# Kernel optimization log

Measured on AMD Instinct MI355X. Metric: run time of the kernel, lower is better.

The kernel has to match this reference:

```python
import jax, jax.numpy as jnp
import numpy as np

N, C_IN, C_OUT, T, V, S = 32, 64, 64, 512, 25, 3
R = C_IN // 2  # rel_channels (in_channel not in (3,9) -> in//rel_reduction=2)
EPS = 1e-5


def setup_inputs() -> dict:
    key = jax.random.key(0)
    ks = jax.random.split(key, 14)
    p = lambda k, shape, s=0.05: jax.random.normal(k, shape, dtype=jnp.float32) * s
    return {
        "x": jax.random.normal(ks[0], (N, C_IN, T, V), dtype=jnp.float32),
        "A": p(ks[1], (S, V, V), 0.2),            # fixed adjacency per subset
        "w1": p(ks[2], (S, R, C_IN)),             # conv1 1x1 per subset
        "b1": p(ks[3], (S, R)),
        "w2": p(ks[4], (S, R, C_IN)),             # conv2 1x1
        "b2": p(ks[5], (S, R)),
        "w3": p(ks[6], (S, C_OUT, C_IN)),         # conv3 1x1 (value)
        "b3": p(ks[7], (S, C_OUT)),
        "w4": p(ks[8], (S, C_OUT, R)),            # conv4 1x1 on relation tensor
        "b4": p(ks[9], (S, C_OUT)),
        "alpha": p(ks[10], (S,), 0.1),            # per-subset scalar (nn.Parameter zeros(1); randomized for non-degenerate test)
        "bn_gamma": jnp.ones((C_OUT,), dtype=jnp.float32),
        "bn_beta": jnp.zeros((C_OUT,), dtype=jnp.float32),
    }


def reference(x, A, w1, b1, w2, b2, w3, b3, w4, b4, alpha, bn_gamma, bn_beta):
    # x: [N,C,T,V]. 1x1 conv commutes with mean over T, so pool first (same math).
    xm = x.mean(axis=2)                                              # [N,C,V]
    q = jnp.einsum('ncv,src->nsrv', xm, w1) + b1[None, :, :, None]   # conv1(x).mean(-2)
    k = jnp.einsum('ncv,src->nsrv', xm, w2) + b2[None, :, :, None]   # conv2(x).mean(-2)
    v = jnp.einsum('nctv,soc->nsotv', x, w3) + b3[None, :, :, None, None]  # conv3(x)
    # outer difference over nodes: [N,S,R,V,V]
    rel = jax.nn.relu(q[..., :, None] - k[..., None, :])
    # conv4 (1x1 over rel channels) * alpha + A[s]
    att = jnp.einsum('nsruv,sor->nsouv', rel, w4) + b4[None, :, :, None, None]
    att = att * alpha[None, :, None, None, None] + A[None, :, None, :, :]  # [N,S,O,V,V]
    # aggregation: einsum('ncuv,nctv->nctu') summed over subsets
    y = jnp.einsum('nsouv,nsotv->notu', att, v)                      # [N,O,T,V]
    # BatchNorm2d in training mode (batch statistics, biased variance)
    mu = y.mean(axis=(0, 2, 3), keepdims=True)
    var = y.var(axis=(0, 2, 3), keepdims=True)
    ybn = (y - mu) * jax.lax.rsqrt(var + EPS) * bn_gamma[None, :, None, None] + bn_beta[None, :, None, None]
    # act(y) + bn(y) + residual (Identity since in_channel == out_channel)
    return jax.nn.relu(y) + ybn + x
```

## Files before the change

kernel.cpp:

```cpp
#include <hip/hip_runtime.h>
#include <hip/hip_bf16.h>

#define XM_OFF   0
#define ATT_OFF  51200
#define SSUM_OFF 3891200
#define SSQ_OFF  3891264
#define SCL_OFF  3891328
#define SHF_OFF  3891392
#define Y_BYTE_OFF  (3891456ull * 4ull)
#define VT_BYTE_OFF (Y_BYTE_OFF + 52428800ull)

#define CONV_SWAP 0

typedef __attribute__((ext_vector_type(8))) short short8;
typedef __attribute__((ext_vector_type(4))) float f32x4;

__device__ __forceinline__ ushort f2bs(float f) {
  __hip_bfloat16 h = __float2bfloat16(f);
  ushort u; __builtin_memcpy(&u, &h, 2); return u;
}
__device__ __forceinline__ float bs2f(ushort u) {
  return __uint_as_float((unsigned)u << 16);
}

__global__ __launch_bounds__(256) void k_xm(const float* __restrict__ x,
                                            float* __restrict__ ws) {
  const int b = blockIdx.x;
  const int tid = threadIdx.x;
  if (b == 0 && tid < 128) ws[SSUM_OFF + tid] = 0.f;
  const float* base = x + (size_t)b * 12800;
  float acc[25];
#pragma unroll
  for (int v = 0; v < 25; ++v) acc[v] = 0.f;
  for (int t = tid; t < 512; t += 256) {
    const float* row = base + t * 25;
#pragma unroll
    for (int v = 0; v < 25; ++v) acc[v] += row[v];
  }
  __shared__ float red[256][25];
#pragma unroll
  for (int v = 0; v < 25; ++v) red[tid][v] = acc[v];
  __syncthreads();
  for (int st = 128; st > 0; st >>= 1) {
    if (tid < st) {
#pragma unroll
      for (int v = 0; v < 25; ++v) red[tid][v] += red[tid + st][v];
    }
    __syncthreads();
  }
  if (tid < 25) ws[XM_OFF + b * 25 + tid] = red[0][tid] * (1.0f / 512.0f);
}

__global__ __launch_bounds__(256) void k_att(const float* __restrict__ ws,
    const float* __restrict__ A, const float* __restrict__ w1, const float* __restrict__ b1,
    const float* __restrict__ w2, const float* __restrict__ b2, const float* __restrict__ w4,
    const float* __restrict__ b4, const float* __restrict__ alpha, float* __restrict__ attg) {
  const int b = blockIdx.x;
  const int n = b / 24; const int r = b % 24; const int s = r >> 3; const int og = r & 7;
  const int tid = threadIdx.x;
  __shared__ float xs[1600];
  __shared__ float qb[800];
  __shared__ float kb[800];
  for (int j = tid; j < 1600; j += 256) xs[j] = ws[XM_OFF + n * 1600 + j];
  __syncthreads();
  for (int i = tid; i < 1600; i += 256) {
    const int half = i / 800;
    const int ii = i % 800;
    const int rr = ii / 25, v = ii % 25;
    const float* w = half ? w2 : w1;
    const float* bb = half ? b2 : b1;
    float acc = bb[s * 32 + rr];
    const float* wr = w + (s * 32 + rr) * 64;
#pragma unroll 8
    for (int c = 0; c < 64; ++c) acc += wr[c] * xs[c * 25 + v];
    (half ? kb : qb)[ii] = acc;
  }
  __syncthreads();
  const float al = alpha[s];
  for (int i = tid; i < 5000; i += 256) {
    const int o2 = i / 625, r2 = i % 625;
    const int u = r2 / 25, v = r2 % 25;
    const int o = og * 8 + o2;
    const float* wr = w4 + (s * 64 + o) * 32;
    float acc = 0.f;
#pragma unroll 8
    for (int rr2 = 0; rr2 < 32; ++rr2) {
      const float d = qb[rr2 * 25 + u] - kb[rr2 * 25 + v];
      acc += wr[rr2] * fmaxf(d, 0.f);
    }
    attg[((size_t)(n * 3 + s) * 64 + o) * 625 + r2] =
        (acc + b4[s * 64 + o]) * al + A[s * 625 + r2];
  }
}

__global__ __launch_bounds__(256) void k_conv3(const float* __restrict__ x,
    const float* __restrict__ w3, const float* __restrict__ b3,
    ushort* __restrict__ vt, int n_base) {
  __shared__ ushort xbf[2][16][64][8];
  __shared__ ushort shv[64 * 256];
  const int tid = threadIdx.x;
  const int nh = blockIdx.x / 50, chunk = blockIdx.x % 50;
  const int n = n_base + nh;
  const int item0 = chunk * 256;

  {
    const float* xb = x + (size_t)n * 819200 + item0 + tid;
    const int col = tid & 15, nt = tid >> 4;
#pragma unroll
    for (int cq = 0; cq < 16; ++cq) {
      const int c0 = cq * 4;
      const float f0 = xb[(size_t)(c0 + 0) * 12800];
      const float f1 = xb[(size_t)(c0 + 1) * 12800];
      const float f2 = xb[(size_t)(c0 + 2) * 12800];
      const float f3 = xb[(size_t)(c0 + 3) * 12800];
      ushort4 p;
      p.x = f2bs(f0); p.y = f2bs(f1); p.z = f2bs(f2); p.w = f2bs(f3);
      const int kb = c0 >> 5;
#if CONV_SWAP == 0
      const int h  = (c0 >> 4) & 1;
      const int kg = (c0 >> 2) & 3;
      *(ushort4*)&xbf[kb][nt][kg * 16 + col][h * 4] = p;
#else
      const int cp = c0 & 31;
      *(ushort4*)&xbf[kb][nt][(cp >> 3) * 16 + col][c0 & 4] = p;
#endif
    }
  }
  __syncthreads();

  const int lane = tid & 63, wid = tid >> 6;
  const int o0 = wid * 16;
  const int orow = o0 + (lane & 15);
  const int kg = lane >> 4;

  short8 afr[3][2];
  float4 b3v[3];
#pragma unroll
  for (int s = 0; s < 3; ++s) {
    const float* wrow = w3 + ((size_t)s * 64 + orow) * 64;
#pragma unroll
    for (int kb2 = 0; kb2 < 2; ++kb2) {
#if CONV_SWAP == 0
      const float4 lo = *(const float4*)(wrow + kb2 * 32 + kg * 4);
      const float4 hi = *(const float4*)(wrow + kb2 * 32 + 16 + kg * 4);
#else
      const float4 lo = *(const float4*)(wrow + kb2 * 32 + kg * 8);
      const float4 hi = *(const float4*)(wrow + kb2 * 32 + kg * 8 + 4);
#endif
      short8 a;
      a[0] = (short)f2bs(lo.x); a[1] = (short)f2bs(lo.y);
      a[2] = (short)f2bs(lo.z); a[3] = (short)f2bs(lo.w);
      a[4] = (short)f2bs(hi.x); a[5] = (short)f2bs(hi.y);
      a[6] = (short)f2bs(hi.z); a[7] = (short)f2bs(hi.w);
      afr[s][kb2] = a;
    }
    b3v[s] = *(const float4*)(b3 + s * 64 + o0 + (lane >> 4) * 4);
  }

  const int obase = o0 + (lane >> 4) * 4;
  const int colit = lane & 15;

  for (int s = 0; s < 3; ++s) {
#pragma unroll
    for (int nt = 0; nt < 16; ++nt) {
      f32x4 acc;
      acc[0] = b3v[s].x; acc[1] = b3v[s].y; acc[2] = b3v[s].z; acc[3] = b3v[s].w;
      const short8 bf0 = *(const short8*)&xbf[0][nt][lane][0];
      const short8 bf1 = *(const short8*)&xbf[1][nt][lane][0];
      acc = __builtin_amdgcn_mfma_f32_16x16x32_bf16(afr[s][0], bf0, acc, 0, 0, 0);
      acc = __builtin_amdgcn_mfma_f32_16x16x32_bf16(afr[s][1], bf1, acc, 0, 0, 0);
      const int item = nt * 16 + colit;
#pragma unroll
      for (int r = 0; r < 4; ++r) {
        const int oo = obase + r;
        shv[oo * 256 + (item ^ ((oo & 7) << 3))] = f2bs(acc[r]);
      }
    }
    __syncthreads();
    {
      const int o = tid >> 2, seg = tid & 3;
      ushort* dst = vt + (((size_t)nh * 3 + s) * 64 + o) * 12800 + item0;
      const ushort* srow = &shv[o * 256];
      const int xr = (o & 7) << 3;
#pragma unroll
      for (int g = 0; g < 8; ++g) {
        const int ib = g * 32 + seg * 8;
        *(int4*)(dst + ib) = *(const int4*)(srow + (ib ^ xr));
      }
    }
    __syncthreads();
  }
}

__global__ __launch_bounds__(256) void k_agg(const ushort* __restrict__ vt,
    const float* __restrict__ attg, float* __restrict__ ssum, float* __restrict__ ssq,
    ushort* __restrict__ yg, int n_base) {
  const int bid = blockIdx.x;
  const int tc = bid & 1, o = (bid >> 1) & 63, nh = bid >> 7;
  const int n = n_base + nh;
  const int t = tc * 256 + threadIdx.x;
  const float* ab = attg + ((size_t)(n * 3) * 64 + o) * 625;
  float acc[25];
#pragma unroll
  for (int u = 0; u < 25; ++u) acc[u] = 0.f;

  for (int s = 0; s < 3; ++s) {
    const ushort* vr = vt + ((((size_t)nh * 3 + s) * 64 + o) * 512 + t) * 25;
    float xv[25];
#pragma unroll
    for (int v = 0; v < 25; ++v) xv[v] = bs2f(vr[v]);
    const float* ar = ab + s * 40000;
#pragma unroll
    for (int u = 0; u < 25; ++u) {
      const float* arr = ar + u * 25;
#pragma unroll
      for (int v = 0; v < 25; ++v) acc[u] = fmaf(arr[v], xv[v], acc[u]);
    }
  }

  ushort* yr = yg + (((size_t)n * 64 + o) * 512 + t) * 25;
  float s1 = 0.f, s2 = 0.f;
#pragma unroll
  for (int u = 0; u < 25; ++u) {
    const float yv = acc[u];
    s1 += yv; s2 += yv * yv;
    yr[u] = f2bs(yv);
  }
#pragma unroll
  for (int off = 32; off > 0; off >>= 1) {
    s1 += __shfl_down(s1, off);
    s2 += __shfl_down(s2, off);
  }
  __shared__ float rs[8];
  const int lane = threadIdx.x & 63, wid = threadIdx.x >> 6;
  if (lane == 0) { rs[wid] = s1; rs[4 + wid] = s2; }
  __syncthreads();
  if (threadIdx.x == 0) {
    atomicAdd(&ssum[o], rs[0] + rs[1] + rs[2] + rs[3]);
    atomicAdd(&ssq[o], rs[4] + rs[5] + rs[6] + rs[7]);
  }
}

__global__ __launch_bounds__(64) void k_stats(const float* __restrict__ ssum,
    const float* __restrict__ ssq, const float* __restrict__ gamma,
    const float* __restrict__ beta, float* __restrict__ scl, float* __restrict__ shf) {
  const int o = threadIdx.x;
  const float inv = 1.0f / 409600.0f;
  const float mu = ssum[o] * inv;
  const float var = ssq[o] * inv - mu * mu;
  const float rstd = rsqrtf(var + 1e-5f);
  const float sc = gamma[o] * rstd;
  scl[o] = sc;
  shf[o] = beta[o] - mu * sc;
}

__global__ __launch_bounds__(256) void k_final(const float* __restrict__ x,
    const ushort* __restrict__ yg, const float* __restrict__ scl,
    const float* __restrict__ shf, float* __restrict__ out) {
  const int stride = gridDim.x * blockDim.x;
  for (int i = blockIdx.x * 256 + threadIdx.x; i < 6553600; i += stride) {
    const int o = (i / 3200) & 63;
    const float sc = scl[o], sh = shf[o];
    const float4 xv = ((const float4*)x)[i];
    const ushort4 yu = ((const ushort4*)yg)[i];
    const float y0 = bs2f(yu.x), y1 = bs2f(yu.y), y2 = bs2f(yu.z), y3 = bs2f(yu.w);
    float4 r;
    r.x = fmaxf(y0, 0.f) + y0 * sc + sh + xv.x;
    r.y = fmaxf(y1, 0.f) + y1 * sc + sh + xv.y;
    r.z = fmaxf(y2, 0.f) + y2 * sc + sh + xv.z;
    r.w = fmaxf(y3, 0.f) + y3 * sc + sh + xv.w;
    ((float4*)out)[i] = r;
  }
}

extern "C" void kernel_launch(void* const* d_in, const int* in_sizes, int n_in,
                              void* d_out, int out_size, void* d_ws, size_t ws_size,
                              hipStream_t stream) {
  const float* x     = (const float*)d_in[0];
  const float* A     = (const float*)d_in[1];
  const float* w1    = (const float*)d_in[2];
  const float* b1    = (const float*)d_in[3];
  const float* w2    = (const float*)d_in[4];
  const float* b2    = (const float*)d_in[5];
  const float* w3    = (const float*)d_in[6];
  const float* b3    = (const float*)d_in[7];
  const float* w4    = (const float*)d_in[8];
  const float* b4    = (const float*)d_in[9];
  const float* alpha = (const float*)d_in[10];
  const float* gamma = (const float*)d_in[11];
  const float* beta  = (const float*)d_in[12];
  float* ws = (float*)d_ws;
  float* attg = ws + ATT_OFF;
  ushort* yg = (ushort*)((char*)d_ws + Y_BYTE_OFF);
  ushort* vtb = (ushort*)((char*)d_ws + VT_BYTE_OFF);
  float* out = (float*)d_out;

  k_xm<<<2048, 256, 0, stream>>>(x, ws);
  k_att<<<768, 256, 0, stream>>>(ws, A, w1, b1, w2, b2, w4, b4, alpha, attg);
  for (int ph = 0; ph < 2; ++ph) {
    const int n_base = ph * 16;
    k_conv3<<<800, 256, 0, stream>>>(x, w3, b3, vtb, n_base);
    k_agg<<<2048, 256, 0, stream>>>(vtb, attg, ws + SSUM_OFF, ws + SSQ_OFF, yg, n_base);
  }
  k_stats<<<1, 64, 0, stream>>>(ws + SSUM_OFF, ws + SSQ_OFF, gamma, beta,
                                ws + SCL_OFF, ws + SHF_OFF);
  k_final<<<2048, 256, 0, stream>>>(x, yg, ws + SCL_OFF, ws + SHF_OFF, out);
}
```

Measured before the change: 471.9 us.

## Rewrite aggregation kernel with bf16 MFMA and LDS-staged V slabs

The per-(n,o) aggregation kernel now loads the attention matrices as bf16 MFMA A-fragments and stages each subset's V slab into shared memory, then computes y with 16x16x32 bf16 MFMA instead of scalar FMAs. Results are transposed through LDS so the y writes are coalesced 16-byte stores, and the BN partial sums are taken from the rounded values. The grid is halved so each block covers all 512 time steps. This trades fp32 accumulation inputs for bf16 attention weights (extra rounding) and adds LDS traffic and barriers. The dead CONV_SWAP preprocessor branch is also removed.

```diff
diff --git a/kernel.cpp b/kernel.cpp
--- a/kernel.cpp
+++ b/kernel.cpp
@@ -9,8 +9,6 @@
 #define SHF_OFF  3891392
 #define Y_BYTE_OFF  (3891456ull * 4ull)
 #define VT_BYTE_OFF (Y_BYTE_OFF + 52428800ull)
-
-#define CONV_SWAP 0
 
 typedef __attribute__((ext_vector_type(8))) short short8;
 typedef __attribute__((ext_vector_type(4))) float f32x4;
@@ -116,14 +114,9 @@
       ushort4 p;
       p.x = f2bs(f0); p.y = f2bs(f1); p.z = f2bs(f2); p.w = f2bs(f3);
       const int kb = c0 >> 5;
-#if CONV_SWAP == 0
       const int h  = (c0 >> 4) & 1;
       const int kg = (c0 >> 2) & 3;
       *(ushort4*)&xbf[kb][nt][kg * 16 + col][h * 4] = p;
-#else
-      const int cp = c0 & 31;
-      *(ushort4*)&xbf[kb][nt][(cp >> 3) * 16 + col][c0 & 4] = p;
-#endif
     }
   }
   __syncthreads();
@@ -140,13 +133,8 @@
     const float* wrow = w3 + ((size_t)s * 64 + orow) * 64;
 #pragma unroll
     for (int kb2 = 0; kb2 < 2; ++kb2) {
-#if CONV_SWAP == 0
       const float4 lo = *(const float4*)(wrow + kb2 * 32 + kg * 4);
       const float4 hi = *(const float4*)(wrow + kb2 * 32 + 16 + kg * 4);
-#else
-      const float4 lo = *(const float4*)(wrow + kb2 * 32 + kg * 8);
-      const float4 hi = *(const float4*)(wrow + kb2 * 32 + kg * 8 + 4);
-#endif
       short8 a;
       a[0] = (short)f2bs(lo.x); a[1] = (short)f2bs(lo.y);
       a[2] = (short)f2bs(lo.z); a[3] = (short)f2bs(lo.w);
@@ -195,36 +183,98 @@
 __global__ __launch_bounds__(256) void k_agg(const ushort* __restrict__ vt,
     const float* __restrict__ attg, float* __restrict__ ssum, float* __restrict__ ssq,
     ushort* __restrict__ yg, int n_base) {
+  __shared__ __align__(16) ushort vs[14336];
   const int bid = blockIdx.x;
-  const int tc = bid & 1, o = (bid >> 1) & 63, nh = bid >> 7;
+  const int o = bid & 63, nh = bid >> 6;
   const int n = n_base + nh;
-  const int t = tc * 256 + threadIdx.x;
-  const float* ab = attg + ((size_t)(n * 3) * 64 + o) * 625;
-  float acc[25];
-#pragma unroll
-  for (int u = 0; u < 25; ++u) acc[u] = 0.f;
-
+  const int tid = threadIdx.x;
+  const int lane = tid & 63, wid = tid >> 6;
+  const int kg = lane >> 4;
+  const int trow = lane & 15;
+
+  short8 afr[3][2];
+#pragma unroll
   for (int s = 0; s < 3; ++s) {
-    const ushort* vr = vt + ((((size_t)nh * 3 + s) * 64 + o) * 512 + t) * 25;
-    float xv[25];
-#pragma unroll
-    for (int v = 0; v < 25; ++v) xv[v] = bs2f(vr[v]);
-    const float* ar = ab + s * 40000;
-#pragma unroll
-    for (int u = 0; u < 25; ++u) {
-      const float* arr = ar + u * 25;
-#pragma unroll
-      for (int v = 0; v < 25; ++v) acc[u] = fmaf(arr[v], xv[v], acc[u]);
-    }
-  }
-
-  ushort* yr = yg + (((size_t)n * 64 + o) * 512 + t) * 25;
+    const float* ab = attg + ((size_t)(n * 3 + s) * 64 + o) * 625;
+#pragma unroll
+    for (int mt = 0; mt < 2; ++mt) {
+      const int u = mt * 16 + (lane & 15);
+      short8 a;
+#pragma unroll
+      for (int i = 0; i < 8; ++i) {
+        const int v = kg * 4 + (i & 3) + ((i >> 2) << 4);
+        float val = (u < 25 && v < 25) ? ab[u * 25 + v] : 0.f;
+        a[i] = (short)f2bs(val);
+      }
+      afr[s][mt] = a;
+    }
+  }
+
+  f32x4 acc0[8], acc1[8];
+#pragma unroll
+  for (int nt = 0; nt < 8; ++nt) {
+    acc0[nt] = (f32x4)0.f; acc1[nt] = (f32x4)0.f;
+  }
+
+  for (int s = 0; s < 3; ++s) {
+    const ushort* vslab = vt + (((size_t)nh * 3 + s) * 64 + o) * 12800;
+    for (int j = tid; j < 1600; j += 256)
+      *(int4*)&vs[j * 8] = *(const int4*)&vslab[j * 8];
+    __syncthreads();
+#pragma unroll
+    for (int nt = 0; nt < 8; ++nt) {
+      const int t = wid * 128 + nt * 16 + trow;
+      short8 b;
+#pragma unroll
+      for (int i = 0; i < 8; ++i) {
+        const int v = kg * 4 + (i & 3) + ((i >> 2) << 4);
+        b[i] = (v < 25) ? (short)vs[t * 25 + v] : (short)0;
+      }
+      acc0[nt] = __builtin_amdgcn_mfma_f32_16x16x32_bf16(afr[s][0], b, acc0[nt], 0, 0, 0);
+      acc1[nt] = __builtin_amdgcn_mfma_f32_16x16x32_bf16(afr[s][1], b, acc1[nt], 0, 0, 0);
+    }
+    __syncthreads();
+  }
+
+#pragma unroll
+  for (int nt = 0; nt < 8; ++nt) {
+    const int t = wid * 128 + nt * 16 + trow;
+#pragma unroll
+    for (int mt = 0; mt < 2; ++mt) {
+      const int u0 = mt * 16 + kg * 4;
+      if (u0 <= 24) {
+        const f32x4 a = mt ? acc1[nt] : acc0[nt];
+        uint2 pk;
+        pk.x = (uint)f2bs(a[0]) | ((uint)f2bs(a[1]) << 16);
+        pk.y = (uint)f2bs(a[2]) | ((uint)f2bs(a[3]) << 16);
+        *(uint2*)&vs[t * 28 + u0] = pk;
+      }
+    }
+  }
+  __syncthreads();
+
   float s1 = 0.f, s2 = 0.f;
-#pragma unroll
-  for (int u = 0; u < 25; ++u) {
-    const float yv = acc[u];
-    s1 += yv; s2 += yv * yv;
-    yr[u] = f2bs(yv);
+  ushort* yslab = yg + ((size_t)(n * 64 + o)) * 12800;
+#pragma unroll
+  for (int k = 0; k < 7; ++k) {
+    const int grp = tid + k * 256;
+    if (grp < 1600) {
+      const int j0 = grp * 8;
+      uint w[4];
+#pragma unroll
+      for (int e = 0; e < 4; ++e) {
+        const int ja = j0 + e * 2, jb = ja + 1;
+        const int ta = ja / 25, ua = ja - ta * 25;
+        const int tb = jb / 25, ub = jb - tb * 25;
+        const ushort wa = vs[ta * 28 + ua];
+        const ushort wb = vs[tb * 28 + ub];
+        w[e] = (uint)wa | ((uint)wb << 16);
+        const float fa = bs2f(wa), fb = bs2f(wb);
+        s1 += fa + fb; s2 += fa * fa + fb * fb;
+      }
+      int4 st; st.x = (int)w[0]; st.y = (int)w[1]; st.z = (int)w[2]; st.w = (int)w[3];
+      *(int4*)&yslab[j0] = st;
+    }
   }
 #pragma unroll
   for (int off = 32; off > 0; off >>= 1) {
@@ -232,10 +282,9 @@
     s2 += __shfl_down(s2, off);
   }
   __shared__ float rs[8];
-  const int lane = threadIdx.x & 63, wid = threadIdx.x >> 6;
   if (lane == 0) { rs[wid] = s1; rs[4 + wid] = s2; }
   __syncthreads();
-  if (threadIdx.x == 0) {
+  if (tid == 0) {
     atomicAdd(&ssum[o], rs[0] + rs[1] + rs[2] + rs[3]);
     atomicAdd(&ssq[o], rs[4] + rs[5] + rs[6] + rs[7]);
   }
@@ -300,7 +349,7 @@
   for (int ph = 0; ph < 2; ++ph) {
     const int n_base = ph * 16;
     k_conv3<<<800, 256, 0, stream>>>(x, w3, b3, vtb, n_base);
-    k_agg<<<2048, 256, 0, stream>>>(vtb, attg, ws + SSUM_OFF, ws + SSQ_OFF, yg, n_base);
+    k_agg<<<1024, 256, 0, stream>>>(vtb, attg, ws + SSUM_OFF, ws + SSQ_OFF, yg, n_base);
   }
   k_stats<<<1, 64, 0, stream>>>(ws + SSUM_OFF, ws + SSQ_OFF, gamma, beta,
                                 ws + SCL_OFF, ws + SHF_OFF);
```

Result: faster. 419.5 us (-11.1%).
